# Optimization experiments

Measured on AMD Instinct MI355X. Metric: run time of the kernel, lower is better.

Reference implementation:

```python
import jax, jax.numpy as jnp
import numpy as np

D, C, H, W = 8, 512, 64, 64


def setup_inputs() -> dict:
    key = jax.random.key(0)
    k1, k2, k3 = jax.random.split(key, 3)
    x = jax.random.normal(k1, (D, C, H, W), dtype=jnp.float32)
    atten = jax.random.normal(k2, (D, C, C), dtype=jnp.float32)
    gamma = jax.random.normal(k3, (1,), dtype=jnp.float32)
    return {"x": x, "atten": atten, "gamma": gamma}


def reference(x, atten, gamma):
    d, c, h, w = x.shape
    q = x.reshape(d, c, h * w)              # q == v == flattened x; k = q^T
    # energy[d, i, j] = <channel_i, channel_j> over spatial positions
    energy = jnp.einsum('din,djn->dij', q, q)
    # max-centering: rowmax - energy (note the sign flip vs standard softmax)
    energy_new = jnp.max(energy, axis=-1, keepdims=True) - energy
    attention = jax.nn.softmax(energy_new, axis=-1)
    attention = jax.nn.softmax(attention + atten, axis=-1)
    # out = attention^T @ v : out[d, j, n] = sum_i attention[d, i, j] * v[d, i, n]
    out = jnp.einsum('dij,din->djn', attention, q).reshape(d, c, h, w)
    return gamma * out + x
```

## Files before the change

### kernel.cpp

```cpp
#include <hip/hip_runtime.h>
#include <hip/hip_bf16.h>

#define DD 8
#define CC 512
#define NN 4096

typedef __bf16 bf16x8 __attribute__((ext_vector_type(8)));
typedef float  f32x4  __attribute__((ext_vector_type(4)));
typedef ushort ush8   __attribute__((ext_vector_type(8)));

__device__ __forceinline__ ushort f2bf(float f) {
  unsigned u = __float_as_uint(f);
  u = (u + 0x7fffu + ((u >> 16) & 1u)) >> 16;
  return (ushort)u;
}
__device__ __forceinline__ float bf2f(ushort h) {
  return __uint_as_float(((unsigned)h) << 16);
}

__device__ __forceinline__ void gl_lds16(const ushort* g, ushort* l) {
  __builtin_amdgcn_global_load_lds(
      (const __attribute__((address_space(1))) void*)g,
      (__attribute__((address_space(3))) void*)l, 16, 0, 0);
}

__global__ __launch_bounds__(256) void k0_convert(
    const float* __restrict__ x, ushort* __restrict__ qh,
    ushort* __restrict__ ql, ushort* __restrict__ qt) {
  int d = blockIdx.z, ct = blockIdx.y, nt = blockIdx.x;
  __shared__ ushort T[64][68];
  int t = threadIdx.x;
  int rr = t >> 4;
  int c4 = (t & 15) * 4;
  const float* xb = x + ((size_t)(d * CC + ct * 64)) * NN + nt * 64;
#pragma unroll
  for (int it = 0; it < 4; ++it) {
    int r = it * 16 + rr;
    float4 v = *(const float4*)(xb + (size_t)r * NN + c4);
    ushort h0 = f2bf(v.x), h1 = f2bf(v.y), h2 = f2bf(v.z), h3 = f2bf(v.w);
    ushort l0 = f2bf(v.x - bf2f(h0)), l1 = f2bf(v.y - bf2f(h1));
    ushort l2 = f2bf(v.z - bf2f(h2)), l3 = f2bf(v.w - bf2f(h3));
    size_t qi = ((size_t)(d * CC + ct * 64 + r)) * NN + nt * 64 + c4;
    *(ushort4*)(qh + qi) = make_ushort4(h0, h1, h2, h3);
    *(ushort4*)(ql + qi) = make_ushort4(l0, l1, l2, l3);
    *(ushort4*)&T[r][c4] = make_ushort4(h0, h1, h2, h3);
  }
  __syncthreads();
#pragma unroll
  for (int it = 0; it < 4; ++it) {
    int nl = it * 16 + rr;
    ushort4 v = make_ushort4(T[c4 + 0][nl], T[c4 + 1][nl], T[c4 + 2][nl], T[c4 + 3][nl]);
    *(ushort4*)(qt + ((size_t)(d * NN + nt * 64 + nl)) * CC + ct * 64 + c4) = v;
  }
}

__global__ __launch_bounds__(256, 2) void k1_gram(
    const ushort* __restrict__ qh, const ushort* __restrict__ ql,
    float* __restrict__ Ep, int ns, int nkk, int ksp) {
  __shared__ ushort As[2][128 * 32];
  __shared__ ushort Bs[2][128 * 32];
  int b = blockIdx.x;
  int s = b % ns;
  int rem = b / ns;
  int tile = rem % 10, d = rem / 10;
  int tm = (int)((0x3221110000ULL >> (tile * 4)) & 15ULL);
  int tn = (int)((0x3323213210ULL >> (tile * 4)) & 15ULL);
  int t = threadIdx.x, lane = t & 63, w = t >> 6;
  int wm = (w >> 1) * 64, wn = (w & 1) * 64;
  int qd = lane >> 4, fr = lane & 15;

  const ushort* srcbase = (w & 1) ? ql : qh;
  int rowblk = (w < 2) ? tm : tn;
  const ushort* gsrc = srcbase +
      ((size_t)(d * CC + rowblk * 128 + (lane >> 2))) * NN +
      (size_t)s * ksp + (lane & 3) * 8;
  ushort* ldst = (w < 2) ? As[w & 1] : Bs[w & 1];

  f32x4 acc[4][4];
#pragma unroll
  for (int i = 0; i < 4; ++i)
#pragma unroll
    for (int j = 0; j < 4; ++j) acc[i][j] = (f32x4){0.f, 0.f, 0.f, 0.f};

  for (int kk = 0; kk < nkk; ++kk) {
    __syncthreads();
    const ushort* g0 = gsrc + (size_t)kk * 32;
#pragma unroll
    for (int c = 0; c < 8; ++c)
      gl_lds16(g0 + (size_t)c * 16 * NN, ldst + c * 512);
    __syncthreads();

    bf16x8 ah[4], al[4];
#pragma unroll
    for (int mi = 0; mi < 4; ++mi) {
      int off = (wm + mi * 16 + fr) * 32 + qd * 8;
      ah[mi] = *(const bf16x8*)&As[0][off];
      al[mi] = *(const bf16x8*)&As[1][off];
    }
#pragma unroll
    for (int ni = 0; ni < 4; ++ni) {
      int off = (wn + ni * 16 + fr) * 32 + qd * 8;
      bf16x8 bh = *(const bf16x8*)&Bs[0][off];
      bf16x8 bl = *(const bf16x8*)&Bs[1][off];
#pragma unroll
      for (int mi = 0; mi < 4; ++mi) {
        acc[mi][ni] = __builtin_amdgcn_mfma_f32_16x16x32_bf16(ah[mi], bh, acc[mi][ni], 0, 0, 0);
        acc[mi][ni] = __builtin_amdgcn_mfma_f32_16x16x32_bf16(ah[mi], bl, acc[mi][ni], 0, 0, 0);
        acc[mi][ni] = __builtin_amdgcn_mfma_f32_16x16x32_bf16(al[mi], bh, acc[mi][ni], 0, 0, 0);
      }
    }
  }

  size_t ebase = ((size_t)(s * DD + d)) * ((size_t)CC * CC);
#pragma unroll
  for (int mi = 0; mi < 4; ++mi) {
    int r0 = tm * 128 + wm + mi * 16 + qd * 4;
#pragma unroll
    for (int ni = 0; ni < 4; ++ni) {
      int c0 = tn * 128 + wn + ni * 16 + fr;
      float* ep = Ep + ebase + (size_t)r0 * CC + c0;
#pragma unroll
      for (int r = 0; r < 4; ++r) ep[(size_t)r * CC] = acc[mi][ni][r];
    }
  }
  if (tm != tn) {
#pragma unroll
    for (int mi = 0; mi < 4; ++mi) {
      int r0 = tm * 128 + wm + mi * 16 + qd * 4;
#pragma unroll
      for (int ni = 0; ni < 4; ++ni) {
        int c0 = tn * 128 + wn + ni * 16 + fr;
        float4 v = make_float4(acc[mi][ni][0], acc[mi][ni][1],
                               acc[mi][ni][2], acc[mi][ni][3]);
        *(float4*)(Ep + ebase + (size_t)c0 * CC + r0) = v;
      }
    }
  }
}

__device__ __forceinline__ float wmin(float v) {
#pragma unroll
  for (int o = 32; o > 0; o >>= 1) v = fminf(v, __shfl_xor(v, o));
  return v;
}
__device__ __forceinline__ float wmax(float v) {
#pragma unroll
  for (int o = 32; o > 0; o >>= 1) v = fmaxf(v, __shfl_xor(v, o));
  return v;
}
__device__ __forceinline__ float wsum(float v) {
#pragma unroll
  for (int o = 32; o > 0; o >>= 1) v += __shfl_xor(v, o);
  return v;
}

__global__ __launch_bounds__(256) void k2_softmax(
    const float* __restrict__ Ep, const float* __restrict__ atten,
    ushort* __restrict__ a2t, int ns) {
  int d = blockIdx.y, i0 = blockIdx.x * 8;
  int t = threadIdx.x, lane = t & 63, w = t >> 6;
  int j8 = lane * 8;
  __shared__ ushort T[8][520];
  const size_t SP = (size_t)DD * CC * CC;

#pragma unroll
  for (int r2 = 0; r2 < 2; ++r2) {
    int ri = w * 2 + r2;
    size_t base = ((size_t)(d * CC + i0 + ri)) * CC + j8;
    f32x4 a0 = (f32x4){0.f, 0.f, 0.f, 0.f};
    f32x4 a1 = (f32x4){0.f, 0.f, 0.f, 0.f};
    for (int s = 0; s < ns; ++s) {
      const float* p = Ep + (size_t)s * SP + base;
      a0 += *(const f32x4*)p;
      a1 += *(const f32x4*)(p + 4);
    }
    float mn = fminf(fminf(fminf(a0[0], a0[1]), fminf(a0[2], a0[3])),
                     fminf(fminf(a1[0], a1[1]), fminf(a1[2], a1[3])));
    mn = wmin(mn);
    float p0 = __expf(mn - a0[0]), p1 = __expf(mn - a0[1]);
    float p2 = __expf(mn - a0[2]), p3 = __expf(mn - a0[3]);
    float p4 = __expf(mn - a1[0]), p5 = __expf(mn - a1[1]);
    float p6 = __expf(mn - a1[2]), p7 = __expf(mn - a1[3]);
    float s1 = wsum(p0 + p1 + p2 + p3 + p4 + p5 + p6 + p7);
    float inv1 = 1.0f / s1;
    const float* ap = atten + base;
    f32x4 t0 = *(const f32x4*)ap;
    f32x4 t1 = *(const f32x4*)(ap + 4);
    float u0 = p0 * inv1 + t0[0], u1 = p1 * inv1 + t0[1];
    float u2 = p2 * inv1 + t0[2], u3 = p3 * inv1 + t0[3];
    float u4 = p4 * inv1 + t1[0], u5 = p5 * inv1 + t1[1];
    float u6 = p6 * inv1 + t1[2], u7 = p7 * inv1 + t1[3];
    float mx = wmax(fmaxf(fmaxf(fmaxf(u0, u1), fmaxf(u2, u3)),
                          fmaxf(fmaxf(u4, u5), fmaxf(u6, u7))));
    float q0 = __expf(u0 - mx), q1 = __expf(u1 - mx);
    float q2 = __expf(u2 - mx), q3 = __expf(u3 - mx);
    float q4 = __expf(u4 - mx), q5 = __expf(u5 - mx);
    float q6 = __expf(u6 - mx), q7 = __expf(u7 - mx);
    float s2 = wsum(q0 + q1 + q2 + q3 + q4 + q5 + q6 + q7);
    float inv2 = 1.0f / s2;
    ush8 o;
    o[0] = f2bf(q0 * inv2); o[1] = f2bf(q1 * inv2);
    o[2] = f2bf(q2 * inv2); o[3] = f2bf(q3 * inv2);
    o[4] = f2bf(q4 * inv2); o[5] = f2bf(q5 * inv2);
    o[6] = f2bf(q6 * inv2); o[7] = f2bf(q7 * inv2);
    *(ush8*)&T[ri][j8] = o;
  }
  __syncthreads();
#pragma unroll
  for (int it = 0; it < 2; ++it) {
    int j = t + it * 256;
    ush8 o;
#pragma unroll
    for (int k = 0; k < 8; ++k) o[k] = T[k][j];
    *(ush8*)&a2t[((size_t)(d * CC + j)) * CC + i0] = o;
  }
}

__global__ __launch_bounds__(256, 2) void k3_out(
    const ushort* __restrict__ a2t, const ushort* __restrict__ qt,
    const float* __restrict__ x, const float* __restrict__ gamma,
    float* __restrict__ out) {
  __shared__ ushort As[128 * 32];
  __shared__ ushort Bs[128 * 32];
  int b = blockIdx.x;
  int nt = b & 31, jt = (b >> 5) & 3, d = b >> 7;
  int t = threadIdx.x, lane = t & 63, w = t >> 6;
  int wj = (w >> 1) * 64, wn2 = (w & 1) * 64;
  int qd = lane >> 4, fr = lane & 15;

  const ushort* src = (w < 2)
      ? (a2t + (size_t)d * CC * CC + (size_t)(jt * 128) * CC)
      : (qt + (size_t)d * NN * CC + (size_t)(nt * 128) * CC);
  ushort* ldst = (w < 2) ? As : Bs;
  int cbase = (w & 1) * 4;
  const ushort* g0 = src + ((size_t)(cbase * 16 + (lane >> 2))) * CC + (lane & 3) * 8;
  ushort* l0 = ldst + cbase * 16 * 32;

  f32x4 acc[4][4];
#pragma unroll
  for (int i = 0; i < 4; ++i)
#pragma unroll
    for (int j = 0; j < 4; ++j) acc[i][j] = (f32x4){0.f, 0.f, 0.f, 0.f};

  for (int kk = 0; kk < CC / 32; ++kk) {
    __syncthreads();
#pragma unroll
    for (int c = 0; c < 4; ++c)
      gl_lds16(g0 + kk * 32 + (size_t)(c * 16) * CC, l0 + c * 512);
    __syncthreads();

    bf16x8 qf[4];
#pragma unroll
    for (int ii = 0; ii < 4; ++ii)
      qf[ii] = *(const bf16x8*)&Bs[(wn2 + ii * 16 + fr) * 32 + qd * 8];
#pragma unroll
    for (int jj = 0; jj < 4; ++jj) {
      bf16x8 af = *(const bf16x8*)&As[(wj + jj * 16 + fr) * 32 + qd * 8];
#pragma unroll
      for (int ii = 0; ii < 4; ++ii)
        acc[ii][jj] = __builtin_amdgcn_mfma_f32_16x16x32_bf16(qf[ii], af, acc[ii][jj], 0, 0, 0);
    }
  }

  float g = gamma[0];
#pragma unroll
  for (int ii = 0; ii < 4; ++ii) {
    int n0 = nt * 128 + wn2 + ii * 16 + qd * 4;
#pragma unroll
    for (int jj = 0; jj < 4; ++jj) {
      int j = jt * 128 + wj + jj * 16 + fr;
      size_t idx = ((size_t)(d * CC + j)) * NN + n0;
      float4 xv = *(const float4*)(x + idx);
      float4 ov = make_float4(g * acc[ii][jj][0] + xv.x,
                              g * acc[ii][jj][1] + xv.y,
                              g * acc[ii][jj][2] + xv.z,
                              g * acc[ii][jj][3] + xv.w);
      *(float4*)(out + idx) = ov;
    }
  }
}

extern "C" void kernel_launch(void* const* d_in, const int* in_sizes, int n_in,
                              void* d_out, int out_size, void* d_ws, size_t ws_size,
                              hipStream_t stream) {
  (void)in_sizes; (void)n_in; (void)out_size;
  const float* x     = (const float*)d_in[0];
  const float* atten = (const float*)d_in[1];
  const float* gamma = (const float*)d_in[2];
  float* out = (float*)d_out;

  char* ws = (char*)d_ws;
  ushort* qh  = (ushort*)(ws);
  ushort* ql  = (ushort*)(ws + 33554432);
  ushort* qt  = (ushort*)(ws + 67108864);
  ushort* a2t = (ushort*)(ws + 100663296);
  float*  Ep  = (float*) (ws + 104857600);

  int ns = (ws_size >= 104857600ULL + 8ULL * 8388608ULL) ? 8 : 4;
  int ksp = NN / ns;
  int nkk = ksp / 32;

  k0_convert<<<dim3(64, 8, 8), 256, 0, stream>>>(x, qh, ql, qt);
  k1_gram   <<<dim3(80 * ns), 256, 0, stream>>>(qh, ql, Ep, ns, nkk, ksp);
  k2_softmax<<<dim3(64, 8), 256, 0, stream>>>(Ep, atten, a2t, ns);
  k3_out    <<<dim3(1024), 256, 0, stream>>>(a2t, qt, x, gamma, out);
}
```

Baseline: 231.1 us.

## Double-buffer LDS tiles in output GEMM and prefetch residual x in epilogue

The output kernel's shared-memory A/B tiles become double-buffered, so the global-to-LDS load for the next K slice is issued before the MFMAs on the current slice. This cuts one barrier per iteration and overlaps load latency with compute. The epilogue also loads the residual x values ahead of time, fetching the next row group while the current one is written. LDS use per block doubles, and the extra prefetched float4 registers add register pressure.

```diff
diff --git a/kernel.cpp b/kernel.cpp
--- a/kernel.cpp
+++ b/kernel.cpp
@@ -216,12 +216,28 @@
   }
 }
 
+#define K3_COMPUTE(BUF)                                                        \
+  {                                                                            \
+    bf16x8 qf[4];                                                              \
+    _Pragma("unroll")                                                          \
+    for (int ii = 0; ii < 4; ++ii)                                             \
+      qf[ii] = *(const bf16x8*)&Bs[BUF][(wn2 + ii * 16 + fr) * 32 + qd * 8];   \
+    _Pragma("unroll")                                                          \
+    for (int jj = 0; jj < 4; ++jj) {                                           \
+      bf16x8 af = *(const bf16x8*)&As[BUF][(wj + jj * 16 + fr) * 32 + qd * 8]; \
+      _Pragma("unroll")                                                        \
+      for (int ii = 0; ii < 4; ++ii)                                           \
+        acc[ii][jj] = __builtin_amdgcn_mfma_f32_16x16x32_bf16(                 \
+            qf[ii], af, acc[ii][jj], 0, 0, 0);                                 \
+    }                                                                          \
+  }
+
 __global__ __launch_bounds__(256, 2) void k3_out(
     const ushort* __restrict__ a2t, const ushort* __restrict__ qt,
     const float* __restrict__ x, const float* __restrict__ gamma,
     float* __restrict__ out) {
-  __shared__ ushort As[128 * 32];
-  __shared__ ushort Bs[128 * 32];
+  __shared__ ushort As[2][128 * 32];
+  __shared__ ushort Bs[2][128 * 32];
   int b = blockIdx.x;
   int nt = b & 31, jt = (b >> 5) & 3, d = b >> 7;
   int t = threadIdx.x, lane = t & 63, w = t >> 6;
@@ -231,10 +247,10 @@
   const ushort* src = (w < 2)
       ? (a2t + (size_t)d * CC * CC + (size_t)(jt * 128) * CC)
       : (qt + (size_t)d * NN * CC + (size_t)(nt * 128) * CC);
-  ushort* ldst = (w < 2) ? As : Bs;
   int cbase = (w & 1) * 4;
   const ushort* g0 = src + ((size_t)(cbase * 16 + (lane >> 2))) * CC + (lane & 3) * 8;
-  ushort* l0 = ldst + cbase * 16 * 32;
+  ushort* lb0 = ((w < 2) ? As[0] : Bs[0]) + cbase * 16 * 32;
+  ushort* lb1 = ((w < 2) ? As[1] : Bs[1]) + cbase * 16 * 32;
 
   f32x4 acc[4][4];
 #pragma unroll
@@ -242,40 +258,60 @@
 #pragma unroll
     for (int j = 0; j < 4; ++j) acc[i][j] = (f32x4){0.f, 0.f, 0.f, 0.f};
 
-  for (int kk = 0; kk < CC / 32; ++kk) {
+#pragma unroll
+  for (int c = 0; c < 4; ++c)
+    gl_lds16(g0 + (size_t)(c * 16) * CC, lb0 + c * 512);
+  __syncthreads();
+
+  for (int kk = 0; kk < CC / 32 - 1; ++kk) {
+    ushort* ln = (kk & 1) ? lb0 : lb1;
+    const ushort* gn = g0 + (size_t)(kk + 1) * 32;
+#pragma unroll
+    for (int c = 0; c < 4; ++c)
+      gl_lds16(gn + (size_t)(c * 16) * CC, ln + c * 512);
+    int cb = kk & 1;
+    K3_COMPUTE(cb);
     __syncthreads();
-#pragma unroll
-    for (int c = 0; c < 4; ++c)
-      gl_lds16(g0 + kk * 32 + (size_t)(c * 16) * CC, l0 + c * 512);
-    __syncthreads();
-
-    bf16x8 qf[4];
-#pragma unroll
-    for (int ii = 0; ii < 4; ++ii)
-      qf[ii] = *(const bf16x8*)&Bs[(wn2 + ii * 16 + fr) * 32 + qd * 8];
+  }
+
+  float4 xp[4];
+  {
+    int n0 = nt * 128 + wn2 + qd * 4;
 #pragma unroll
     for (int jj = 0; jj < 4; ++jj) {
-      bf16x8 af = *(const bf16x8*)&As[(wj + jj * 16 + fr) * 32 + qd * 8];
-#pragma unroll
-      for (int ii = 0; ii < 4; ++ii)
-        acc[ii][jj] = __builtin_amdgcn_mfma_f32_16x16x32_bf16(qf[ii], af, acc[ii][jj], 0, 0, 0);
-    }
-  }
+      int j = jt * 128 + wj + jj * 16 + fr;
+      xp[jj] = *(const float4*)(x + ((size_t)(d * CC + j)) * NN + n0);
+    }
+  }
+  K3_COMPUTE(1);
 
   float g = gamma[0];
 #pragma unroll
   for (int ii = 0; ii < 4; ++ii) {
+    float4 xn[4];
+    if (ii < 3) {
+      int n0n = nt * 128 + wn2 + (ii + 1) * 16 + qd * 4;
+#pragma unroll
+      for (int jj = 0; jj < 4; ++jj) {
+        int j = jt * 128 + wj + jj * 16 + fr;
+        xn[jj] = *(const float4*)(x + ((size_t)(d * CC + j)) * NN + n0n);
+      }
+    }
     int n0 = nt * 128 + wn2 + ii * 16 + qd * 4;
 #pragma unroll
     for (int jj = 0; jj < 4; ++jj) {
       int j = jt * 128 + wj + jj * 16 + fr;
       size_t idx = ((size_t)(d * CC + j)) * NN + n0;
-      float4 xv = *(const float4*)(x + idx);
-      float4 ov = make_float4(g * acc[ii][jj][0] + xv.x,
-                              g * acc[ii][jj][1] + xv.y,
-                              g * acc[ii][jj][2] + xv.z,
-                              g * acc[ii][jj][3] + xv.w);
+      float4 xvv = xp[jj];
+      float4 ov = make_float4(g * acc[ii][jj][0] + xvv.x,
+                              g * acc[ii][jj][1] + xvv.y,
+                              g * acc[ii][jj][2] + xvv.z,
+                              g * acc[ii][jj][3] + xvv.w);
       *(float4*)(out + idx) = ov;
+    }
+    if (ii < 3) {
+#pragma unroll
+      for (int jj = 0; jj < 4; ++jj) xp[jj] = xn[jj];
     }
   }
 }
```

New measurement: 235.2 us. About the same (+1.7%).

## Load MFMA operands directly from global memory, drop LDS staging and barriers

Applied to the files above, without the earlier changes.

The gram and output GEMM kernels stop staging tiles in LDS through global_load_lds and syncthreads. Each wave now loads its bf16 fragments straight from global memory into registers, relying on L2/L1 for reuse across waves. The output kernel also doubles its N tile to 256 per block, halves the grid, and software-prefetches the residual x values. Block indices are remapped so the batch index varies fastest, and the gram kernel's occupancy hint is raised to 3. The risk is more redundant global/L2 traffic, since waves sharing a tile no longer share an LDS copy, and more register pressure from the larger accumulator set.

```diff
diff --git a/kernel.cpp b/kernel.cpp
--- a/kernel.cpp
+++ b/kernel.cpp
@@ -16,12 +16,6 @@
 }
 __device__ __forceinline__ float bf2f(ushort h) {
   return __uint_as_float(((unsigned)h) << 16);
-}
-
-__device__ __forceinline__ void gl_lds16(const ushort* g, ushort* l) {
-  __builtin_amdgcn_global_load_lds(
-      (const __attribute__((address_space(1))) void*)g,
-      (__attribute__((address_space(3))) void*)l, 16, 0, 0);
 }
 
 __global__ __launch_bounds__(256) void k0_convert(
@@ -54,11 +48,9 @@
   }
 }
 
-__global__ __launch_bounds__(256, 2) void k1_gram(
+__global__ __launch_bounds__(256, 3) void k1_gram(
     const ushort* __restrict__ qh, const ushort* __restrict__ ql,
     float* __restrict__ Ep, int ns, int nkk, int ksp) {
-  __shared__ ushort As[2][128 * 32];
-  __shared__ ushort Bs[2][128 * 32];
   int b = blockIdx.x;
   int s = b % ns;
   int rem = b / ns;
@@ -69,12 +61,12 @@
   int wm = (w >> 1) * 64, wn = (w & 1) * 64;
   int qd = lane >> 4, fr = lane & 15;
 
-  const ushort* srcbase = (w & 1) ? ql : qh;
-  int rowblk = (w < 2) ? tm : tn;
-  const ushort* gsrc = srcbase +
-      ((size_t)(d * CC + rowblk * 128 + (lane >> 2))) * NN +
-      (size_t)s * ksp + (lane & 3) * 8;
-  ushort* ldst = (w < 2) ? As[w & 1] : Bs[w & 1];
+  size_t offA = ((size_t)(d * CC + tm * 128 + wm + fr)) * NN + (size_t)s * ksp + qd * 8;
+  size_t offB = ((size_t)(d * CC + tn * 128 + wn + fr)) * NN + (size_t)s * ksp + qd * 8;
+  const ushort* hA = qh + offA;
+  const ushort* lA = ql + offA;
+  const ushort* hB = qh + offB;
+  const ushort* lB = ql + offB;
 
   f32x4 acc[4][4];
 #pragma unroll
@@ -82,33 +74,28 @@
 #pragma unroll
     for (int j = 0; j < 4; ++j) acc[i][j] = (f32x4){0.f, 0.f, 0.f, 0.f};
 
+#pragma unroll 2
   for (int kk = 0; kk < nkk; ++kk) {
-    __syncthreads();
-    const ushort* g0 = gsrc + (size_t)kk * 32;
-#pragma unroll
-    for (int c = 0; c < 8; ++c)
-      gl_lds16(g0 + (size_t)c * 16 * NN, ldst + c * 512);
-    __syncthreads();
-
-    bf16x8 ah[4], al[4];
+    int ko = kk * 32;
+    bf16x8 ah[4], al[4], bh[4], bl[4];
 #pragma unroll
     for (int mi = 0; mi < 4; ++mi) {
-      int off = (wm + mi * 16 + fr) * 32 + qd * 8;
-      ah[mi] = *(const bf16x8*)&As[0][off];
-      al[mi] = *(const bf16x8*)&As[1][off];
+      ah[mi] = *(const bf16x8*)(hA + (size_t)(mi * 16) * NN + ko);
+      al[mi] = *(const bf16x8*)(lA + (size_t)(mi * 16) * NN + ko);
     }
 #pragma unroll
     for (int ni = 0; ni < 4; ++ni) {
-      int off = (wn + ni * 16 + fr) * 32 + qd * 8;
-      bf16x8 bh = *(const bf16x8*)&Bs[0][off];
-      bf16x8 bl = *(const bf16x8*)&Bs[1][off];
+      bh[ni] = *(const bf16x8*)(hB + (size_t)(ni * 16) * NN + ko);
+      bl[ni] = *(const bf16x8*)(lB + (size_t)(ni * 16) * NN + ko);
+    }
+#pragma unroll
+    for (int ni = 0; ni < 4; ++ni)
 #pragma unroll
       for (int mi = 0; mi < 4; ++mi) {
-        acc[mi][ni] = __builtin_amdgcn_mfma_f32_16x16x32_bf16(ah[mi], bh, acc[mi][ni], 0, 0, 0);
-        acc[mi][ni] = __builtin_amdgcn_mfma_f32_16x16x32_bf16(ah[mi], bl, acc[mi][ni], 0, 0, 0);
-        acc[mi][ni] = __builtin_amdgcn_mfma_f32_16x16x32_bf16(al[mi], bh, acc[mi][ni], 0, 0, 0);
+        acc[mi][ni] = __builtin_amdgcn_mfma_f32_16x16x32_bf16(ah[mi], bh[ni], acc[mi][ni], 0, 0, 0);
+        acc[mi][ni] = __builtin_amdgcn_mfma_f32_16x16x32_bf16(ah[mi], bl[ni], acc[mi][ni], 0, 0, 0);
+        acc[mi][ni] = __builtin_amdgcn_mfma_f32_16x16x32_bf16(al[mi], bh[ni], acc[mi][ni], 0, 0, 0);
       }
-    }
   }
 
   size_t ebase = ((size_t)(s * DD + d)) * ((size_t)CC * CC);
@@ -157,7 +144,8 @@
 __global__ __launch_bounds__(256) void k2_softmax(
     const float* __restrict__ Ep, const float* __restrict__ atten,
     ushort* __restrict__ a2t, int ns) {
-  int d = blockIdx.y, i0 = blockIdx.x * 8;
+  int d = blockIdx.x & 7;
+  int i0 = (blockIdx.x >> 3) * 8;
   int t = threadIdx.x, lane = t & 63, w = t >> 6;
   int j8 = lane * 8;
   __shared__ ushort T[8][520];
@@ -220,62 +208,74 @@
     const ushort* __restrict__ a2t, const ushort* __restrict__ qt,
     const float* __restrict__ x, const float* __restrict__ gamma,
     float* __restrict__ out) {
-  __shared__ ushort As[128 * 32];
-  __shared__ ushort Bs[128 * 32];
   int b = blockIdx.x;
-  int nt = b & 31, jt = (b >> 5) & 3, d = b >> 7;
+  int d = b & 7, jt = (b >> 3) & 3, ntp = b >> 5;
   int t = threadIdx.x, lane = t & 63, w = t >> 6;
-  int wj = (w >> 1) * 64, wn2 = (w & 1) * 64;
+  int wj = (w >> 1) * 64;
+  int wn2 = (w & 1) * 128;
   int qd = lane >> 4, fr = lane & 15;
 
-  const ushort* src = (w < 2)
-      ? (a2t + (size_t)d * CC * CC + (size_t)(jt * 128) * CC)
-      : (qt + (size_t)d * NN * CC + (size_t)(nt * 128) * CC);
-  ushort* ldst = (w < 2) ? As : Bs;
-  int cbase = (w & 1) * 4;
-  const ushort* g0 = src + ((size_t)(cbase * 16 + (lane >> 2))) * CC + (lane & 3) * 8;
-  ushort* l0 = ldst + cbase * 16 * 32;
-
-  f32x4 acc[4][4];
-#pragma unroll
-  for (int i = 0; i < 4; ++i)
+  const ushort* aA = a2t + ((size_t)(d * CC + jt * 128 + wj + fr)) * CC + qd * 8;
+  const ushort* aB = qt + ((size_t)(d * NN + ntp * 256 + wn2 + fr)) * CC + qd * 8;
+
+  f32x4 acc[8][4];
+#pragma unroll
+  for (int i = 0; i < 8; ++i)
 #pragma unroll
     for (int j = 0; j < 4; ++j) acc[i][j] = (f32x4){0.f, 0.f, 0.f, 0.f};
 
-  for (int kk = 0; kk < CC / 32; ++kk) {
-    __syncthreads();
-#pragma unroll
-    for (int c = 0; c < 4; ++c)
-      gl_lds16(g0 + kk * 32 + (size_t)(c * 16) * CC, l0 + c * 512);
-    __syncthreads();
-
-    bf16x8 qf[4];
-#pragma unroll
-    for (int ii = 0; ii < 4; ++ii)
-      qf[ii] = *(const bf16x8*)&Bs[(wn2 + ii * 16 + fr) * 32 + qd * 8];
+#pragma unroll 2
+  for (int kk = 0; kk < 16; ++kk) {
+    int ko = kk * 32;
+    bf16x8 qf[8], af[4];
+#pragma unroll
+    for (int ii = 0; ii < 8; ++ii)
+      qf[ii] = *(const bf16x8*)(aB + (size_t)(ii * 16) * CC + ko);
+#pragma unroll
+    for (int jj = 0; jj < 4; ++jj)
+      af[jj] = *(const bf16x8*)(aA + (size_t)(jj * 16) * CC + ko);
+#pragma unroll
+    for (int jj = 0; jj < 4; ++jj)
+#pragma unroll
+      for (int ii = 0; ii < 8; ++ii)
+        acc[ii][jj] = __builtin_amdgcn_mfma_f32_16x16x32_bf16(
+            qf[ii], af[jj], acc[ii][jj], 0, 0, 0);
+  }
+
+  float g = gamma[0];
+  int n0b = ntp * 256 + wn2 + qd * 4;
+  int jb = jt * 128 + wj + fr;
+  float4 xp[4], xq[4];
+#pragma unroll
+  for (int jj = 0; jj < 4; ++jj) {
+    size_t rb = ((size_t)(d * CC + jb + jj * 16)) * NN;
+    xp[jj] = *(const float4*)(x + rb + n0b);
+    xq[jj] = *(const float4*)(x + rb + n0b + 16);
+  }
+
+#pragma unroll
+  for (int ii = 0; ii < 8; ++ii) {
+    float4 xn[4];
+    if (ii < 6) {
+#pragma unroll
+      for (int jj = 0; jj < 4; ++jj)
+        xn[jj] = *(const float4*)(x + ((size_t)(d * CC + jb + jj * 16)) * NN +
+                                  n0b + (ii + 2) * 16);
+    }
 #pragma unroll
     for (int jj = 0; jj < 4; ++jj) {
-      bf16x8 af = *(const bf16x8*)&As[(wj + jj * 16 + fr) * 32 + qd * 8];
-#pragma unroll
-      for (int ii = 0; ii < 4; ++ii)
-        acc[ii][jj] = __builtin_amdgcn_mfma_f32_16x16x32_bf16(qf[ii], af, acc[ii][jj], 0, 0, 0);
-    }
-  }
-
-  float g = gamma[0];
-#pragma unroll
-  for (int ii = 0; ii < 4; ++ii) {
-    int n0 = nt * 128 + wn2 + ii * 16 + qd * 4;
-#pragma unroll
-    for (int jj = 0; jj < 4; ++jj) {
-      int j = jt * 128 + wj + jj * 16 + fr;
-      size_t idx = ((size_t)(d * CC + j)) * NN + n0;
-      float4 xv = *(const float4*)(x + idx);
-      float4 ov = make_float4(g * acc[ii][jj][0] + xv.x,
-                              g * acc[ii][jj][1] + xv.y,
-                              g * acc[ii][jj][2] + xv.z,
-                              g * acc[ii][jj][3] + xv.w);
-      *(float4*)(out + idx) = ov;
+      size_t idx = ((size_t)(d * CC + jb + jj * 16)) * NN + n0b + ii * 16;
+      *(float4*)(out + idx) = make_float4(g * acc[ii][jj][0] + xp[jj].x,
+                                          g * acc[ii][jj][1] + xp[jj].y,
+                                          g * acc[ii][jj][2] + xp[jj].z,
+                                          g * acc[ii][jj][3] + xp[jj].w);
+    }
+    if (ii < 6) {
+#pragma unroll
+      for (int jj = 0; jj < 4; ++jj) { xp[jj] = xq[jj]; xq[jj] = xn[jj]; }
+    } else if (ii == 6) {
+#pragma unroll
+      for (int jj = 0; jj < 4; ++jj) xp[jj] = xq[jj];
     }
   }
 }
@@ -302,6 +302,6 @@
 
   k0_convert<<<dim3(64, 8, 8), 256, 0, stream>>>(x, qh, ql, qt);
   k1_gram   <<<dim3(80 * ns), 256, 0, stream>>>(qh, ql, Ep, ns, nkk, ksp);
-  k2_softmax<<<dim3(64, 8), 256, 0, stream>>>(Ep, atten, a2t, ns);
-  k3_out    <<<dim3(1024), 256, 0, stream>>>(a2t, qt, x, gamma, out);
-}
+  k2_softmax<<<dim3(512), 256, 0, stream>>>(Ep, atten, a2t, ns);
+  k3_out    <<<dim3(512), 256, 0, stream>>>(a2t, qt, x, gamma, out);
+}
```

Result: slower. 309.7 us (+34.0%).
